# Optimization experiments

Measured on AMD Instinct MI355X. Metric: run time of the kernel, lower is better.

Reference implementation:

```python
import jax, jax.numpy as jnp
import numpy as np

# ---- static config (mirrors cfg in torch module) ----
CAM_C = 256
OUT_C = 64
IMG_H, IMG_W = 256, 704
DS = 16
FH, FW = IMG_H // DS, IMG_W // DS  # 16, 44
XB = (-51.2, 51.2, 0.8)
YB = (-51.2, 51.2, 0.8)
ZB = (-10.0, 10.0, 20.0)
DB = (1.0, 60.0, 1.0)
D_BINS = int((DB[1] - DB[0]) / DB[2])  # 59
NX = int((XB[1] - XB[0]) / XB[2])      # 128
NY = int((YB[1] - YB[0]) / YB[2])      # 128
NZ = int((ZB[1] - ZB[0]) / ZB[2])      # 1


def _frustum():
    # [D, FH, FW, 3] of (pixel_x, pixel_y, depth)
    ds = DB[0] + DB[2] * jnp.arange(D_BINS, dtype=jnp.float32)
    ds = jnp.broadcast_to(ds[:, None, None], (D_BINS, FH, FW))
    xs = jnp.broadcast_to(jnp.linspace(0.0, IMG_W - 1, FW, dtype=jnp.float32)[None, None, :], (D_BINS, FH, FW))
    ys = jnp.broadcast_to(jnp.linspace(0.0, IMG_H - 1, FH, dtype=jnp.float32)[None, :, None], (D_BINS, FH, FW))
    return jnp.stack([xs, ys, ds], axis=-1)


def setup_inputs() -> dict:
    key = jax.random.key(0)
    ks = jax.random.split(key, 4)
    B, N = 2, 6
    x = jax.random.normal(ks[0], (B, N, CAM_C, FH, FW), jnp.float32)
    # camera->ego base rotation: ego_x = cam_z, ego_y = -cam_x, ego_z = -cam_y
    base = np.array([[0, 0, 1], [-1, 0, 0], [0, -1, 0]], np.float32)
    rots = np.zeros((B, N, 3, 3), np.float32)
    for i, yaw in enumerate(np.linspace(0.0, 2 * np.pi, N, endpoint=False)):
        c, s = np.cos(yaw), np.sin(yaw)
        Rz = np.array([[c, -s, 0], [s, c, 0], [0, 0, 1]], np.float32)
        rots[:, i] = Rz @ base
    trans = np.asarray(jax.random.normal(ks[1], (B, N, 3)), np.float32) * 1.5
    K = np.array([[400.0, 0.0, IMG_W / 2.0], [0.0, 400.0, IMG_H / 2.0], [0.0, 0.0, 1.0]], np.float32)
    intrins = np.broadcast_to(K, (B, N, 3, 3)).copy()
    depth_w = jax.random.normal(ks[2], (D_BINS + OUT_C, CAM_C, 1, 1), jnp.float32) * 0.02
    depth_b = jnp.zeros((D_BINS + OUT_C,), jnp.float32)
    return dict(x=x, rots=jnp.asarray(rots), trans=jnp.asarray(trans),
                intrins=jnp.asarray(intrins), depth_w=depth_w, depth_b=depth_b)


def reference(x, rots, trans, intrins, depth_w, depth_b):
    B, N = x.shape[0], x.shape[1]
    # depth_net: 1x1 conv == channel matmul
    w = depth_w[:, :, 0, 0]  # [D+C, CAM_C]
    feat = jnp.einsum('bnchw,oc->bnohw', x, w) + depth_b[None, None, :, None, None]
    depth = jax.nn.softmax(feat[:, :, :D_BINS], axis=2)        # [B,N,D,FH,FW]
    ctx = feat[:, :, D_BINS:]                                  # [B,N,C,FH,FW]
    # lift: outer product context x depth  -> [B,N,D,FH,FW,C]
    outer = ctx[:, :, :, None] * depth[:, :, None]             # [B,N,C,D,FH,FW]
    outer = jnp.transpose(outer, (0, 1, 3, 4, 5, 2))

    # geometry: unproject frustum to ego frame
    fr = _frustum()
    pts = jnp.concatenate([fr[..., :2] * fr[..., 2:3], fr[..., 2:3]], axis=-1)  # [D,FH,FW,3]
    comb = rots @ jnp.linalg.inv(intrins)                      # [B,N,3,3]
    geom = jnp.einsum('bnij,dhwj->bndhwi', comb, pts) + trans[:, :, None, None, None, :]

    # voxelize
    dx = jnp.array([XB[2], YB[2], ZB[2]], jnp.float32)
    bx = jnp.array([XB[0] + XB[2] / 2.0, YB[0] + YB[2] / 2.0, ZB[0] + ZB[2] / 2.0], jnp.float32)
    coords = jnp.floor((geom - (bx - dx / 2.0)) / dx).astype(jnp.int32)  # [B,N,D,FH,FW,3]

    Np = B * N * D_BINS * FH * FW
    coords = coords.reshape(Np, 3)
    feats = outer.reshape(Np, OUT_C)
    kept = ((coords[:, 0] >= 0) & (coords[:, 0] < NX) &
            (coords[:, 1] >= 0) & (coords[:, 1] < NY) &
            (coords[:, 2] >= 0) & (coords[:, 2] < NZ))
    batch_ix = jnp.repeat(jnp.arange(B, dtype=jnp.int32), N * D_BINS * FH * FW)
    ranks = batch_ix * (NX * NY * NZ) + coords[:, 0] + coords[:, 1] * NX + coords[:, 2] * (NX * NY)
    ranks = jnp.where(kept, ranks, 0)                 # out-of-grid -> dummy seg 0 with zero feats
    feats = feats * kept[:, None].astype(feats.dtype)
    # sort+cumsum-diff+scatter in the original == segment sum over voxel ranks
    flat = jax.ops.segment_sum(feats, ranks, num_segments=B * NZ * NY * NX)  # [B*nz*ny*nx, C]
    bev = flat.reshape(B, NZ, NY, NX, OUT_C)
    bev = jnp.transpose(bev, (0, 4, 1, 2, 3)).sum(axis=2)  # [B, C, NY, NX]
    return bev


if __name__ == '__main__':
    out = reference(**setup_inputs())
    print(out.shape, out.dtype)
```

## Files before the change

kernel.cpp:

```cpp
#include <hip/hip_runtime.h>
#include <hip/hip_bf16.h>
#include <math.h>

#define B_   2
#define N_   6
#define CC   256
#define OCH  64
#define DBN  59
#define FH_  16
#define FW_  44
#define PXI  (FH_*FW_)
#define NPIX (B_*N_*PXI)
#define NPTS (B_*N_*DBN*PXI)
#define NX_  128
#define NY_  128
#define NCELL (B_*NY_*NX_)
#define NOUT 123
#define OUTSZ (B_*OCH*NY_*NX_)
#define TCH  32
#define CONV_BLOCKS 264

#define XSTEP (703.0f/43.0f)
#define YSTEP (255.0f/15.0f)

__device__ __forceinline__ void comb_cam(const float* __restrict__ R,
                                         const float* __restrict__ K,
                                         float* __restrict__ out9) {
    float a = K[0], b = K[1], c = K[2];
    float d = K[3], e = K[4], f = K[5];
    float g = K[6], h = K[7], k = K[8];
    float A  =  __fsub_rn(__fmul_rn(e, k), __fmul_rn(f, h));
    float Bc = -__fsub_rn(__fmul_rn(d, k), __fmul_rn(f, g));
    float Cc =  __fsub_rn(__fmul_rn(d, h), __fmul_rn(e, g));
    float det = __fadd_rn(__fadd_rn(__fmul_rn(a, A), __fmul_rn(b, Bc)),
                          __fmul_rn(c, Cc));
    float inv[9];
    inv[0] = __fdiv_rn(A, det);
    inv[1] = __fdiv_rn(-__fsub_rn(__fmul_rn(b, k), __fmul_rn(c, h)), det);
    inv[2] = __fdiv_rn( __fsub_rn(__fmul_rn(b, f), __fmul_rn(c, e)), det);
    inv[3] = __fdiv_rn(Bc, det);
    inv[4] = __fdiv_rn( __fsub_rn(__fmul_rn(a, k), __fmul_rn(c, g)), det);
    inv[5] = __fdiv_rn(-__fsub_rn(__fmul_rn(a, f), __fmul_rn(c, d)), det);
    inv[6] = __fdiv_rn(Cc, det);
    inv[7] = __fdiv_rn(-__fsub_rn(__fmul_rn(a, h), __fmul_rn(b, g)), det);
    inv[8] = __fdiv_rn( __fsub_rn(__fmul_rn(a, e), __fmul_rn(b, d)), det);
    for (int r = 0; r < 3; ++r)
        for (int cc = 0; cc < 3; ++cc) {
            float s =        __fmul_rn(R[r*3+0], inv[0*3+cc]);
            s = __fadd_rn(s, __fmul_rn(R[r*3+1], inv[1*3+cc]));
            s = __fadd_rn(s, __fmul_rn(R[r*3+2], inv[2*3+cc]));
            out9[r*3 + cc] = s;
        }
}

__global__ __launch_bounds__(256) void k_conv(
        const float* __restrict__ x, const float* __restrict__ wgt,
        const float* __restrict__ bias,
        float* __restrict__ dlog, float* __restrict__ ctx_ws,
        float2* __restrict__ msum, unsigned* __restrict__ cellofs,
        float4* __restrict__ zfill) {
    __shared__ float xs[CC * 64];
    const int t = threadIdx.x;
    const int gid = blockIdx.x * 256 + t;
    const int stride = CONV_BLOCKS * 256;
    for (int i = gid; i < NCELL; i += stride) cellofs[i] = 0u;
    if (zfill) {
        for (int i = gid; i < OUTSZ / 4; i += stride)
            zfill[i] = make_float4(0.f, 0.f, 0.f, 0.f);
    }

    const int pg = blockIdx.x >> 1;
    const int half = blockIdx.x & 1;
    const int pix0 = pg * 64;
    const int bn = pix0 / PXI;
    const int q0 = pix0 - bn * PXI;
    const float* xb = x + (size_t)bn * CC * PXI + q0;

    {
        const int p0 = (t & 15) * 4;
        const int cbase = t >> 4;
        #pragma unroll
        for (int r = 0; r < 16; ++r) {
            const int c = r * 16 + cbase;
            const float4 v = *(const float4*)(xb + (size_t)c * PXI + p0);
            *(float4*)&xs[c * 64 + p0] = v;
        }
    }
    __syncthreads();

    const int w = t >> 6;
    const int lane = t & 63;
    const int o0 = __builtin_amdgcn_readfirstlane(half * 62 + w * 16);
    const int lim = half ? NOUT : 62;

    const float* wp[16];
    #pragma unroll
    for (int kk = 0; kk < 16; ++kk) {
        int oc = o0 + kk; if (oc > NOUT - 1) oc = NOUT - 1;
        wp[kk] = wgt + (size_t)oc * CC;
    }
    float acc[16];
    #pragma unroll
    for (int kk = 0; kk < 16; ++kk) acc[kk] = 0.f;

    #pragma unroll 4
    for (int c = 0; c < CC; ++c) {
        const float xv = xs[c * 64 + lane];
        #pragma unroll
        for (int kk = 0; kk < 16; ++kk)
            acc[kk] = fmaf(xv, wp[kk][c], acc[kk]);
    }

    float av[16];
    #pragma unroll
    for (int kk = 0; kk < 16; ++kk) {
        const int o = o0 + kk;
        if (o >= lim) break;
        const float a = acc[kk] + bias[o];
        av[kk] = a;
        if (o < DBN) dlog[(size_t)o * NPIX + pix0 + lane] = a;
        else         ctx_ws[(size_t)(pix0 + lane) * OCH + (o - DBN)] = a;
    }

    __syncthreads();
    if (half == 0) {
        #pragma unroll
        for (int kk = 0; kk < 16; ++kk) {
            const int o = o0 + kk;
            if (o >= lim) break;
            if (o < DBN) xs[o * 64 + lane] = av[kk];
        }
    }
    __syncthreads();
    if (half == 0 && t < 64) {
        float m = -1e30f;
        #pragma unroll
        for (int d = 0; d < DBN; ++d) m = fmaxf(m, xs[d * 64 + t]);
        float s = 0.f;
        #pragma unroll
        for (int d = 0; d < DBN; ++d) s += expf(xs[d * 64 + t] - m);
        msum[pix0 + t] = make_float2(m, 1.0f / s);
    }
}

__global__ __launch_bounds__(256) void k_geom(
        const float* __restrict__ rots, const float* __restrict__ intrins,
        const float* __restrict__ trans,
        unsigned short* __restrict__ cell16, unsigned* __restrict__ cellofs) {
    __shared__ float combs[B_ * N_ * 9];
    __shared__ float trs[B_ * N_ * 3];
    const int t = threadIdx.x;
    if (t < B_ * N_) comb_cam(rots + t * 9, intrins + t * 9, &combs[t * 9]);
    if (t < B_ * N_ * 3) trs[t] = trans[t];
    __syncthreads();

    const int pt = blockIdx.x * 256 + t;
    const int q  = pt % PXI;
    const int r  = pt / PXI;
    const int dq = r % DBN;
    const int bn = r / DBN;
    const int hq = q / FW_;
    const int wq = q - hq * FW_;
    const int bq = bn / N_;

    const float* cb = &combs[bn * 9];
    const float t0 = trs[bn*3+0], t1 = trs[bn*3+1], t2 = trs[bn*3+2];

    const float dsv = __fadd_rn(1.0f, (float)dq);
    const float xsv = __fmul_rn((float)wq, XSTEP);
    const float ysv = __fmul_rn((float)hq, YSTEP);
    const float px = __fmul_rn(xsv, dsv);
    const float py = __fmul_rn(ysv, dsv);
    const float pz = dsv;
    float gx = __fadd_rn(__fadd_rn(__fmul_rn(cb[0], px), __fmul_rn(cb[1], py)),
                         __fmul_rn(cb[2], pz));
    float gy = __fadd_rn(__fadd_rn(__fmul_rn(cb[3], px), __fmul_rn(cb[4], py)),
                         __fmul_rn(cb[5], pz));
    float gz = __fadd_rn(__fadd_rn(__fmul_rn(cb[6], px), __fmul_rn(cb[7], py)),
                         __fmul_rn(cb[8], pz));
    gx = __fadd_rn(gx, t0);
    gy = __fadd_rn(gy, t1);
    gz = __fadd_rn(gz, t2);

    const float bxv = -50.8f;
    const float lbx = __fsub_rn(bxv, 0.4f);
    const float lbz = -10.0f;
    const int cx = (int)floorf(__fdiv_rn(__fsub_rn(gx, lbx), 0.8f));
    const int cy = (int)floorf(__fdiv_rn(__fsub_rn(gy, lbx), 0.8f));
    const int cz = (int)floorf(__fdiv_rn(__fsub_rn(gz, lbz), 20.0f));

    int c = -1;
    if (cx >= 0 && cx < NX_ && cy >= 0 && cy < NY_ && cz == 0)
        c = bq * (NY_ * NX_) + cy * NX_ + cx;
    cell16[pt] = (c >= 0) ? (unsigned short)c : (unsigned short)0xFFFFu;

    const int lane = t & 63;
    unsigned long long active = __ballot(c >= 0);
    while (active) {
        const int leader = (int)__ffsll((unsigned long long)active) - 1;
        const int lc = __shfl(c, leader);
        const unsigned long long same = __ballot(c == lc);
        if (lane == leader)
            atomicAdd(&cellofs[lc], (unsigned)__popcll(same));
        active &= ~same;
    }
}

__global__ __launch_bounds__(1024) void k_scan(unsigned* __restrict__ cellofs) {
    __shared__ unsigned lds[2][1024];
    const int t = threadIdx.x;
    uint4 u[8];
    const uint4* src4 = (const uint4*)cellofs + (size_t)t * 8;
    #pragma unroll
    for (int i = 0; i < 8; ++i) u[i] = src4[i];
    unsigned vv[32];
    unsigned run = 0;
    #pragma unroll
    for (int i = 0; i < 8; ++i) {
        vv[i*4+0] = run; run += u[i].x;
        vv[i*4+1] = run; run += u[i].y;
        vv[i*4+2] = run; run += u[i].z;
        vv[i*4+3] = run; run += u[i].w;
    }
    lds[0][t] = run;
    __syncthreads();
    int src = 0;
    for (int off = 1; off < 1024; off <<= 1) {
        unsigned val = lds[src][t];
        if (t >= off) val += lds[src][t - off];
        lds[1 - src][t] = val;
        __syncthreads();
        src = 1 - src;
    }
    const unsigned base = (t == 0) ? 0u : lds[src][t - 1];
    uint4* dst4 = (uint4*)cellofs + (size_t)t * 8;
    #pragma unroll
    for (int i = 0; i < 8; ++i) {
        uint4 w;
        w.x = base + vv[i*4+0];
        w.y = base + vv[i*4+1];
        w.z = base + vv[i*4+2];
        w.w = base + vv[i*4+3];
        dst4[i] = w;
    }
}

__global__ __launch_bounds__(256) void k_fill(
        const unsigned short* __restrict__ cell16,
        const float* __restrict__ dlog, const float2* __restrict__ msum,
        unsigned* __restrict__ cellofs, uint2* __restrict__ srt) {
    const int pt = blockIdx.x * 256 + threadIdx.x;
    const unsigned cc = cell16[pt];
    const int c = (cc == 0xFFFFu) ? -1 : (int)cc;
    const int lane = threadIdx.x & 63;

    unsigned slot = 0;
    unsigned long long active = __ballot(c >= 0);
    while (active) {
        const int leader = (int)__ffsll((unsigned long long)active) - 1;
        const int lc = __shfl(c, leader);
        const unsigned long long same = __ballot(c == lc);
        unsigned b0 = 0;
        if (lane == leader)
            b0 = atomicAdd(&cellofs[lc], (unsigned)__popcll(same));
        b0 = __shfl(b0, leader);
        if (c == lc)
            slot = b0 + (unsigned)__popcll(same & ((1ULL << lane) - 1ULL));
        active &= ~same;
    }

    if (c >= 0) {
        const int q  = pt % PXI;
        const int r  = pt / PXI;
        const int dq = r % DBN;
        const int bn = r / DBN;
        const int pix = bn * PXI + q;
        const float2 ms = msum[pix];
        const float w = expf(dlog[(size_t)dq * NPIX + pix] - ms.x) * ms.y;
        srt[slot] = make_uint2(((unsigned)c << 14) | (unsigned)pix,
                               __float_as_uint(w));
    }
}

template <int MODE>
__device__ __forceinline__ void flush_cell(float* __restrict__ dst, unsigned cell,
                                           int ch, float acc, bool use_atomic) {
    float* p;
    if (MODE == 0) {
        p = &dst[((size_t)cell << 6) + ch];
    } else {
        const int b  = (int)(cell >> 14);
        const int cy = (int)((cell >> 7) & 127u);
        const int cx = (int)(cell & 127u);
        p = &dst[(((size_t)(b * OCH + ch)) * NY_ + cy) * NX_ + cx];
    }
    if (use_atomic) atomicAdd(p, acc);
    else            *p = acc;
}

template <int MODE>
__global__ __launch_bounds__(256) void k_gather(
        const unsigned* __restrict__ cellofs, const uint2* __restrict__ srt,
        const float* __restrict__ ctx_ws, float* __restrict__ dst) {
    const int wid = __builtin_amdgcn_readfirstlane(
                        (blockIdx.x * 256 + threadIdx.x) >> 6);
    const int ch = threadIdx.x & 63;
    const unsigned K = cellofs[NCELL - 1];
    unsigned i = (unsigned)wid * TCH;
    if (i >= K) return;
    const unsigned s1 = (i + TCH < K) ? (i + TCH) : K;

    unsigned cur = srt[i].x >> 14;
    float acc = 0.f;
    bool flushed = false;

    while (i + 8 <= s1) {
        uint2 r8[8]; float v8[8];
        #pragma unroll
        for (int j = 0; j < 8; ++j) r8[j] = srt[i + j];
        #pragma unroll
        for (int j = 0; j < 8; ++j)
            v8[j] = ctx_ws[(size_t)(r8[j].x & 0x3FFFu) * OCH + ch];
        #pragma unroll
        for (int j = 0; j < 8; ++j) {
            const unsigned c = r8[j].x >> 14;
            if (c != cur) {
                flush_cell<MODE>(dst, cur, ch, acc, !flushed);
                flushed = true;
                acc = 0.f;
                cur = c;
            }
            acc = fmaf(__uint_as_float(r8[j].y), v8[j], acc);
        }
        i += 8;
    }
    while (i < s1) {
        const uint2 rr = srt[i];
        const float vv = ctx_ws[(size_t)(rr.x & 0x3FFFu) * OCH + ch];
        const unsigned c = rr.x >> 14;
        if (c != cur) {
            flush_cell<MODE>(dst, cur, ch, acc, !flushed);
            flushed = true;
            acc = 0.f;
            cur = c;
        }
        acc = fmaf(__uint_as_float(rr.y), vv, acc);
        ++i;
    }
    flush_cell<MODE>(dst, cur, ch, acc, true);
}

__global__ __launch_bounds__(256) void k_transpose(
        const float* __restrict__ tmp, float* __restrict__ out) {
    __shared__ float tile[64 * 65];
    const int t = threadIdx.x;
    const int w = t >> 6;
    const int lane = t & 63;
    const int b = blockIdx.x >> 8;
    const int c0 = (blockIdx.x & 255) * 64;

    #pragma unroll
    for (int r = 0; r < 16; ++r) {
        const int row = r * 4 + w;
        const float v = tmp[((size_t)(b * (NY_ * NX_) + c0 + row) << 6) + lane];
        tile[lane * 65 + row] = v;
    }
    __syncthreads();
    #pragma unroll
    for (int r = 0; r < 16; ++r) {
        const int chv = r * 4 + w;
        out[((size_t)(b * OCH + chv) * (NY_ * NX_)) + c0 + lane] =
            tile[chv * 65 + lane];
    }
}

extern "C" void kernel_launch(void* const* d_in, const int* in_sizes, int n_in,
                              void* d_out, int out_size, void* d_ws, size_t ws_size,
                              hipStream_t stream) {
    const float* x       = (const float*)d_in[0];
    const float* rots    = (const float*)d_in[1];
    const float* trans   = (const float*)d_in[2];
    const float* intrins = (const float*)d_in[3];
    const float* depth_w = (const float*)d_in[4];
    const float* depth_b = (const float*)d_in[5];
    float* out = (float*)d_out;
    float* ws = (float*)d_ws;

    const int gblocks = (NPTS / TCH + 3) / 4;

    const size_t NEED_TMP_PATH = 14669824;

    if (ws_size >= NEED_TMP_PATH) {
        float* tmp      = ws;
        float* dlog     = ws;
        unsigned short* cell16 = (unsigned short*)(ws + 524288);
        float2* msum    = (float2*)(ws + 786432);
        float* ctx_ws   = ws + 2097152;
        unsigned* cellofs = (unsigned*)(ws + 2637824);
        uint2* srt      = (uint2*)(ws + 2670592);

        k_conv<<<CONV_BLOCKS, 256, 0, stream>>>(x, depth_w, depth_b, dlog,
                                                ctx_ws, msum, cellofs, nullptr);
        k_geom<<<NPTS / 256, 256, 0, stream>>>(rots, intrins, trans,
                                               cell16, cellofs);
        k_scan<<<1, 1024, 0, stream>>>(cellofs);
        k_fill<<<NPTS / 256, 256, 0, stream>>>(cell16, dlog, msum, cellofs, srt);
        hipMemsetAsync(tmp, 0, (size_t)NCELL * OCH * sizeof(float), stream);
        k_gather<0><<<gblocks, 256, 0, stream>>>(cellofs, srt, ctx_ws, tmp);
        k_transpose<<<512, 256, 0, stream>>>(tmp, out);
    } else {
        float* dlog     = ws;
        float* ctx_ws   = ws + 498432;
        float2* msum    = (float2*)(ws + 1039104);
        unsigned* cellofs = (unsigned*)(ws + 1056000);
        unsigned short* cell16 = (unsigned short*)(ws + 1088768);
        uint2* srt      = (uint2*)(ws + 1337984);

        k_conv<<<CONV_BLOCKS, 256, 0, stream>>>(x, depth_w, depth_b, dlog,
                                                ctx_ws, msum, cellofs,
                                                (float4*)out);
        k_geom<<<NPTS / 256, 256, 0, stream>>>(rots, intrins, trans,
                                               cell16, cellofs);
        k_scan<<<1, 1024, 0, stream>>>(cellofs);
        k_fill<<<NPTS / 256, 256, 0, stream>>>(cell16, dlog, msum, cellofs, srt);
        k_gather<1><<<gblocks, 256, 0, stream>>>(cellofs, srt, ctx_ws, out);
    }
}
```

Measured before the change: 178.3 us.

## Split depth-net conv over input channels with separate reduction kernel

The 1x1 conv is split across NK chunks of input channels, giving more blocks (1056 for NK=4) with smaller LDS footprints. A new reduce kernel sums the partials, adds bias, writes dlog and ctx, and computes the softmax max/sum. The small-workspace direct-to-output gather path is removed, so the tmp+transpose path is always used. This trades one extra kernel launch and partial-sum traffic through global memory for better occupancy and parallelism in the conv.

```diff
diff --git a/kernel.cpp b/kernel.cpp
--- a/kernel.cpp
+++ b/kernel.cpp
@@ -18,7 +18,6 @@
 #define NOUT 123
 #define OUTSZ (B_*OCH*NY_*NX_)
 #define TCH  32
-#define CONV_BLOCKS 264
 
 #define XSTEP (703.0f/43.0f)
 #define YSTEP (255.0f/15.0f)
@@ -53,21 +52,120 @@
         }
 }
 
-__global__ __launch_bounds__(256) void k_conv(
+template <int NK>
+__global__ __launch_bounds__(256) void k_conv_split(
+        const float* __restrict__ x, const float* __restrict__ wgt,
+        float* __restrict__ parts, unsigned* __restrict__ cellofs) {
+    constexpr int KC = CC / NK;
+    __shared__ float xs[KC * 64];
+    const int t = threadIdx.x;
+    const int gid = blockIdx.x * 256 + t;
+    const int stride = gridDim.x * 256;
+    for (int i = gid; i < NCELL; i += stride) cellofs[i] = 0u;
+
+    const int kc   = blockIdx.x % NK;
+    const int half = (blockIdx.x / NK) & 1;
+    const int pg   = blockIdx.x / (2 * NK);
+    const int pix0 = pg * 64;
+    const int bn = pix0 / PXI;
+    const int q0 = pix0 - bn * PXI;
+    const float* xb = x + (size_t)bn * CC * PXI + (size_t)(kc * KC) * PXI + q0;
+
+    {
+        const int p0 = (t & 15) * 4;
+        const int cbase = t >> 4;
+        #pragma unroll
+        for (int r = 0; r < KC / 16; ++r) {
+            const int c = r * 16 + cbase;
+            const float4 v = *(const float4*)(xb + (size_t)c * PXI + p0);
+            *(float4*)&xs[c * 64 + p0] = v;
+        }
+    }
+    __syncthreads();
+
+    const int w = t >> 6;
+    const int lane = t & 63;
+    const int o0 = __builtin_amdgcn_readfirstlane(half * 62 + w * 16);
+    const int lim = half ? NOUT : 62;
+
+    const float* wp[16];
+    #pragma unroll
+    for (int kk = 0; kk < 16; ++kk) {
+        int oc = o0 + kk; if (oc > NOUT - 1) oc = NOUT - 1;
+        wp[kk] = wgt + (size_t)oc * CC + kc * KC;
+    }
+    float acc[16];
+    #pragma unroll
+    for (int kk = 0; kk < 16; ++kk) acc[kk] = 0.f;
+
+    #pragma unroll 4
+    for (int c = 0; c < KC; ++c) {
+        const float xv = xs[c * 64 + lane];
+        #pragma unroll
+        for (int kk = 0; kk < 16; ++kk)
+            acc[kk] = fmaf(xv, wp[kk][c], acc[kk]);
+    }
+
+    #pragma unroll
+    for (int kk = 0; kk < 16; ++kk) {
+        const int o = o0 + kk;
+        if (o >= lim) break;
+        parts[((size_t)kc * NOUT + o) * NPIX + pix0 + lane] = acc[kk];
+    }
+}
+
+template <int NK>
+__global__ __launch_bounds__(256) void k_reduce(
+        const float* __restrict__ parts, const float* __restrict__ bias,
+        float* __restrict__ dlog, float* __restrict__ ctx_ws,
+        float2* __restrict__ msum) {
+    __shared__ float lds[NOUT * 65];
+    const int t = threadIdx.x;
+    const int w = t >> 6;
+    const int lane = t & 63;
+    const int pix0 = blockIdx.x * 64;
+
+    #pragma unroll
+    for (int j = 0; j < 31; ++j) {
+        const int o = w * 31 + j;
+        if (o >= NOUT) break;
+        float s = parts[(size_t)o * NPIX + pix0 + lane];
+        #pragma unroll
+        for (int k = 1; k < NK; ++k)
+            s += parts[((size_t)k * NOUT + o) * NPIX + pix0 + lane];
+        s += bias[o];
+        lds[o * 65 + lane] = s;
+        if (o < DBN) dlog[(size_t)o * NPIX + pix0 + lane] = s;
+    }
+    __syncthreads();
+
+    if (t < 64) {
+        float m = -1e30f;
+        #pragma unroll
+        for (int d = 0; d < DBN; ++d) m = fmaxf(m, lds[d * 65 + t]);
+        float s = 0.f;
+        #pragma unroll
+        for (int d = 0; d < DBN; ++d) s += expf(lds[d * 65 + t] - m);
+        msum[pix0 + t] = make_float2(m, 1.0f / s);
+    }
+
+    const int ch = t & 63;
+    const int pq = t >> 6;
+    #pragma unroll
+    for (int px = pq; px < 64; px += 4)
+        ctx_ws[(size_t)(pix0 + px) * OCH + ch] = lds[(DBN + ch) * 65 + px];
+}
+
+__global__ __launch_bounds__(256) void k_conv_mono(
         const float* __restrict__ x, const float* __restrict__ wgt,
         const float* __restrict__ bias,
         float* __restrict__ dlog, float* __restrict__ ctx_ws,
-        float2* __restrict__ msum, unsigned* __restrict__ cellofs,
-        float4* __restrict__ zfill) {
+        float2* __restrict__ msum, unsigned* __restrict__ cellofs) {
     __shared__ float xs[CC * 64];
     const int t = threadIdx.x;
     const int gid = blockIdx.x * 256 + t;
-    const int stride = CONV_BLOCKS * 256;
+    const int stride = gridDim.x * 256;
     for (int i = gid; i < NCELL; i += stride) cellofs[i] = 0u;
-    if (zfill) {
-        for (int i = gid; i < OUTSZ / 4; i += stride)
-            zfill[i] = make_float4(0.f, 0.f, 0.f, 0.f);
-    }
 
     const int pg = blockIdx.x >> 1;
     const int half = blockIdx.x & 1;
@@ -282,26 +380,16 @@
     }
 }
 
-template <int MODE>
-__device__ __forceinline__ void flush_cell(float* __restrict__ dst, unsigned cell,
+__device__ __forceinline__ void flush_cell(float* __restrict__ tmp, unsigned cell,
                                            int ch, float acc, bool use_atomic) {
-    float* p;
-    if (MODE == 0) {
-        p = &dst[((size_t)cell << 6) + ch];
-    } else {
-        const int b  = (int)(cell >> 14);
-        const int cy = (int)((cell >> 7) & 127u);
-        const int cx = (int)(cell & 127u);
-        p = &dst[(((size_t)(b * OCH + ch)) * NY_ + cy) * NX_ + cx];
-    }
-    if (use_atomic) atomicAdd(p, acc);
-    else            *p = acc;
-}
-
-template <int MODE>
+    float* dst = &tmp[((size_t)cell << 6) + ch];
+    if (use_atomic) atomicAdd(dst, acc);
+    else            *dst = acc;
+}
+
 __global__ __launch_bounds__(256) void k_gather(
         const unsigned* __restrict__ cellofs, const uint2* __restrict__ srt,
-        const float* __restrict__ ctx_ws, float* __restrict__ dst) {
+        const float* __restrict__ ctx_ws, float* __restrict__ tmp) {
     const int wid = __builtin_amdgcn_readfirstlane(
                         (blockIdx.x * 256 + threadIdx.x) >> 6);
     const int ch = threadIdx.x & 63;
@@ -325,7 +413,7 @@
         for (int j = 0; j < 8; ++j) {
             const unsigned c = r8[j].x >> 14;
             if (c != cur) {
-                flush_cell<MODE>(dst, cur, ch, acc, !flushed);
+                flush_cell(tmp, cur, ch, acc, !flushed);
                 flushed = true;
                 acc = 0.f;
                 cur = c;
@@ -339,7 +427,7 @@
         const float vv = ctx_ws[(size_t)(rr.x & 0x3FFFu) * OCH + ch];
         const unsigned c = rr.x >> 14;
         if (c != cur) {
-            flush_cell<MODE>(dst, cur, ch, acc, !flushed);
+            flush_cell(tmp, cur, ch, acc, !flushed);
             flushed = true;
             acc = 0.f;
             cur = c;
@@ -347,7 +435,7 @@
         acc = fmaf(__uint_as_float(rr.y), vv, acc);
         ++i;
     }
-    flush_cell<MODE>(dst, cur, ch, acc, true);
+    flush_cell(tmp, cur, ch, acc, true);
 }
 
 __global__ __launch_bounds__(256) void k_transpose(
@@ -386,43 +474,39 @@
     float* out = (float*)d_out;
     float* ws = (float*)d_ws;
 
+    float* tmp      = ws;
+    float* dlog     = ws;
+    unsigned short* cell16 = (unsigned short*)(ws + 524288);
+    float2* msum    = (float2*)(ws + 786432);
+    float* ctx_ws   = ws + 2097152;
+    unsigned* cellofs = (unsigned*)(ws + 2637824);
+    uint2* srt      = (uint2*)(ws + 2670592);
+    float* parts    = ws + 3667456;
+
+    const size_t BASE = 14669824;
+    const size_t PART1 = (size_t)NOUT * NPIX * 4;
     const int gblocks = (NPTS / TCH + 3) / 4;
 
-    const size_t NEED_TMP_PATH = 14669824;
-
-    if (ws_size >= NEED_TMP_PATH) {
-        float* tmp      = ws;
-        float* dlog     = ws;
-        unsigned short* cell16 = (unsigned short*)(ws + 524288);
-        float2* msum    = (float2*)(ws + 786432);
-        float* ctx_ws   = ws + 2097152;
-        unsigned* cellofs = (unsigned*)(ws + 2637824);
-        uint2* srt      = (uint2*)(ws + 2670592);
-
-        k_conv<<<CONV_BLOCKS, 256, 0, stream>>>(x, depth_w, depth_b, dlog,
-                                                ctx_ws, msum, cellofs, nullptr);
-        k_geom<<<NPTS / 256, 256, 0, stream>>>(rots, intrins, trans,
-                                               cell16, cellofs);
-        k_scan<<<1, 1024, 0, stream>>>(cellofs);
-        k_fill<<<NPTS / 256, 256, 0, stream>>>(cell16, dlog, msum, cellofs, srt);
-        hipMemsetAsync(tmp, 0, (size_t)NCELL * OCH * sizeof(float), stream);
-        k_gather<0><<<gblocks, 256, 0, stream>>>(cellofs, srt, ctx_ws, tmp);
-        k_transpose<<<512, 256, 0, stream>>>(tmp, out);
+    if (ws_size >= BASE + 4 * PART1) {
+        k_conv_split<4><<<132 * 2 * 4, 256, 0, stream>>>(x, depth_w,
+                                                         parts, cellofs);
+        k_reduce<4><<<132, 256, 0, stream>>>(parts, depth_b, dlog, ctx_ws,
+                                             msum);
+    } else if (ws_size >= BASE + 2 * PART1) {
+        k_conv_split<2><<<132 * 2 * 2, 256, 0, stream>>>(x, depth_w,
+                                                         parts, cellofs);
+        k_reduce<2><<<132, 256, 0, stream>>>(parts, depth_b, dlog, ctx_ws,
+                                             msum);
     } else {
-        float* dlog     = ws;
-        float* ctx_ws   = ws + 498432;
-        float2* msum    = (float2*)(ws + 1039104);
-        unsigned* cellofs = (unsigned*)(ws + 1056000);
-        unsigned short* cell16 = (unsigned short*)(ws + 1088768);
-        uint2* srt      = (uint2*)(ws + 1337984);
-
-        k_conv<<<CONV_BLOCKS, 256, 0, stream>>>(x, depth_w, depth_b, dlog,
-                                                ctx_ws, msum, cellofs,
-                                                (float4*)out);
-        k_geom<<<NPTS / 256, 256, 0, stream>>>(rots, intrins, trans,
-                                               cell16, cellofs);
-        k_scan<<<1, 1024, 0, stream>>>(cellofs);
-        k_fill<<<NPTS / 256, 256, 0, stream>>>(cell16, dlog, msum, cellofs, srt);
-        k_gather<1><<<gblocks, 256, 0, stream>>>(cellofs, srt, ctx_ws, out);
-    }
-}
+        k_conv_mono<<<264, 256, 0, stream>>>(x, depth_w, depth_b, dlog,
+                                             ctx_ws, msum, cellofs);
+    }
+
+    k_geom<<<NPTS / 256, 256, 0, stream>>>(rots, intrins, trans,
+                                           cell16, cellofs);
+    k_scan<<<1, 1024, 0, stream>>>(cellofs);
+    k_fill<<<NPTS / 256, 256, 0, stream>>>(cell16, dlog, msum, cellofs, srt);
+    hipMemsetAsync(tmp, 0, (size_t)NCELL * OCH * sizeof(float), stream);
+    k_gather<<<gblocks, 256, 0, stream>>>(cellofs, srt, ctx_ws, tmp);
+    k_transpose<<<512, 256, 0, stream>>>(tmp, out);
+}
```

Result: no change. 175.3 us (-1.7%).
